# Kernel optimization log

Measured on AMD Instinct MI355X. Metric: run time of the kernel, lower is better.

## Reference

```python
import jax, jax.numpy as jnp
import numpy as np

B, L, C = 2048, 2048, 16
F = L // 2                 # num_freqs = 1024
H = 4 * F                  # multi_factor * num_freqs = 4096
P = int(len(np.unique(L // np.arange(1, F + 1))))  # n patch sizes = 88
SCALE = 0.02
NOISE_EPS = 0.01


def setup_inputs() -> dict:
    key = jax.random.key(0)
    ks = jax.random.split(key, 10)
    return {
        "x": jax.random.normal(ks[0], (B, L, C), jnp.float32),
        "w_start": SCALE * jax.random.normal(ks[1], (C, 1), jnp.float32),
        "b_start": SCALE * jax.random.normal(ks[2], (1,), jnp.float32),
        "w1": SCALE * jax.random.normal(ks[3], (2, F, H), jnp.float32),
        "b1": SCALE * jax.random.normal(ks[4], (2, H), jnp.float32),
        "w2": SCALE * jax.random.normal(ks[5], (2, H, F), jnp.float32),
        "b2": SCALE * jax.random.normal(ks[6], (2, F), jnp.float32),
        "w_gate": SCALE * jax.random.normal(ks[7], (F, P), jnp.float32),
        "w_noise": SCALE * jax.random.normal(ks[8], (F, P), jnp.float32),
        "noise_z": jax.random.normal(ks[9], (B, P), jnp.float32),
        "top_k": 3,
    }


def reference(x, w_start, b_start, w1, b1, w2, b2, w_gate, w_noise, noise_z, top_k):
    # start_fc: [B, L, C] -> [B, L, 1] -> [B, 1, L]
    v = (jnp.einsum("blc,co->blo", x, w_start) + b_start).transpose(0, 2, 1)
    # rfft (ortho), drop DC bin -> [B, 1, F] complex
    xf = jnp.fft.rfft(v, axis=-1, norm="ortho")[:, :, 1:]
    xr, xi = jnp.real(xf), jnp.imag(xf)
    # complex 2-layer MLP in frequency domain
    o1r = jax.nn.relu(jnp.einsum("bdi,io->bdo", xr, w1[0]) - jnp.einsum("bdi,io->bdo", xi, w1[1]) + b1[0])
    o1i = jax.nn.relu(jnp.einsum("bdi,io->bdo", xi, w1[0]) + jnp.einsum("bdi,io->bdo", xr, w1[1]) + b1[1])
    o2r = jnp.einsum("bdo,of->bdf", o1r, w2[0]) - jnp.einsum("bdo,of->bdf", o1i, w2[1]) + b2[0]
    o2i = jnp.einsum("bdo,of->bdf", o1i, w2[0]) + jnp.einsum("bdo,of->bdf", o1r, w2[1]) + b2[1]
    amp = jnp.sqrt(o2r * o2r + o2i * o2i)[:, 0, :]  # [B, F]
    # router logits with (training) noise injection
    clean_logits = amp @ w_gate                      # [B, P]
    noise_std = jax.nn.softplus(amp @ w_noise) + NOISE_EPS
    logits = clean_logits + noise_z * noise_std
    # top-k -> softmax over top-k -> scatter into sparse gates
    top_w, top_i = jax.lax.top_k(logits, top_k)
    top_w = jax.nn.softmax(top_w, axis=-1)
    rows = jnp.arange(logits.shape[0])[:, None]
    gates = jnp.zeros_like(logits).at[rows, top_i].set(top_w)
    return gates
```

## Files before the change

kernel.cpp:

```cpp
#include <hip/hip_runtime.h>
#include <hip/hip_bf16.h>
#include <math.h>

#define B_DIM 2048
#define L_DIM 2048
#define F_DIM 1024
#define H_DIM 4096
#define P_DIM 88

typedef unsigned short u16;
typedef short bf16x8 __attribute__((ext_vector_type(8)));
typedef float f32x4 __attribute__((ext_vector_type(4)));

__device__ __forceinline__ u16 f2bf(float x) {
    unsigned u = __float_as_uint(x);
    return (u16)((u + 0x7fffu + ((u >> 16) & 1u)) >> 16);
}
__device__ __forceinline__ float bf2f(u16 h) {
    return __uint_as_float(((unsigned)h) << 16);
}

__device__ __forceinline__ void gload_lds16(const void* g, void* l) {
    unsigned loff = (unsigned)(uintptr_t)l;
    __builtin_amdgcn_global_load_lds(
        reinterpret_cast<const __attribute__((address_space(1))) void*>(
            reinterpret_cast<uintptr_t>(g)),
        reinterpret_cast<__attribute__((address_space(3))) void*>(loff),
        16, 0, 0);
}

__global__ __launch_bounds__(256) void fft_kernel(
    const float* __restrict__ x, const float* __restrict__ w_start,
    const float* __restrict__ b_start, u16* __restrict__ A1)
{
    __shared__ float re[2048];
    __shared__ float im[2048];
    __shared__ float twr[1024];
    __shared__ float twi[1024];
    int b = blockIdx.x;
    const size_t row0 = (size_t)(2 * b) * 2048;

    const float4* wp = (const float4*)w_start;
    float4 w0 = wp[0], w1 = wp[1], w2 = wp[2], w3 = wp[3];
    float bs = b_start[0];

    for (int i = threadIdx.x; i < 1024; i += 256) {
        float ang = -6.283185307179586f * ((float)i / 2048.0f);
        sincosf(ang, &twi[i], &twr[i]);
    }

    for (int l = threadIdx.x; l < 2048; l += 256) {
        const float4* xp0 = (const float4*)(x + (row0 + l) * 16);
        const float4* xp1 = (const float4*)(x + (row0 + 2048 + l) * 16);
        float4 a0 = xp0[0], a1 = xp0[1], a2 = xp0[2], a3 = xp0[3];
        float4 c0 = xp1[0], c1 = xp1[1], c2 = xp1[2], c3 = xp1[3];
        float va = bs, vb = bs;
        va += a0.x * w0.x + a0.y * w0.y + a0.z * w0.z + a0.w * w0.w;
        va += a1.x * w1.x + a1.y * w1.y + a1.z * w1.z + a1.w * w1.w;
        va += a2.x * w2.x + a2.y * w2.y + a2.z * w2.z + a2.w * w2.w;
        va += a3.x * w3.x + a3.y * w3.y + a3.z * w3.z + a3.w * w3.w;
        vb += c0.x * w0.x + c0.y * w0.y + c0.z * w0.z + c0.w * w0.w;
        vb += c1.x * w1.x + c1.y * w1.y + c1.z * w1.z + c1.w * w1.w;
        vb += c2.x * w2.x + c2.y * w2.y + c2.z * w2.z + c2.w * w2.w;
        vb += c3.x * w3.x + c3.y * w3.y + c3.z * w3.z + c3.w * w3.w;
        unsigned j = __brev((unsigned)l) >> 21;
        re[j] = va;
        im[j] = vb;
    }
    __syncthreads();

    for (int s = 1; s <= 11; s++) {
        int half = 1 << (s - 1);
        for (int t = threadIdx.x; t < 1024; t += 256) {
            int j = t & (half - 1);
            int base = (t >> (s - 1)) << s;
            int idx = j << (11 - s);
            float wr = twr[idx], wi = twi[idx];
            int i0 = base + j, i1 = i0 + half;
            float br = re[i1], bi = im[i1];
            float tr = br * wr - bi * wi;
            float ti = br * wi + bi * wr;
            float ar = re[i0], ai = im[i0];
            re[i0] = ar + tr; im[i0] = ai + ti;
            re[i1] = ar - tr; im[i1] = ai - ti;
        }
        __syncthreads();
    }

    const float sc = 0.5f * 0.022097086912079612f;
    u16* r0 = A1 + (size_t)(2 * b) * 4096;
    u16* r1 = r0 + 4096;
    for (int t = threadIdx.x; t < 1024; t += 256) {
        int k = t + 1;
        int nk = 2048 - k;
        float Zr = re[k], Zi = im[k], Yr = re[nk], Yi = im[nk];
        float Ar = (Zr + Yr) * sc;
        float Ai = (Zi - Yi) * sc;
        float Br = (Zi + Yi) * sc;
        float Bi = (Yr - Zr) * sc;
        u16 h, lo;
        h = f2bf(Ar); lo = f2bf(Ar - bf2f(h)); r0[t] = h; r0[1024 + t] = lo;
        h = f2bf(Ai); lo = f2bf(Ai - bf2f(h)); r0[2048 + t] = h; r0[3072 + t] = lo;
        h = f2bf(Br); lo = f2bf(Br - bf2f(h)); r1[t] = h; r1[1024 + t] = lo;
        h = f2bf(Bi); lo = f2bf(Bi - bf2f(h)); r1[2048 + t] = h; r1[3072 + t] = lo;
    }
}

__global__ __launch_bounds__(256) void conv_bt_kernel(
    const float* __restrict__ w, u16* __restrict__ BT, int Kc, int Nh)
{
    __shared__ float t0[32][33];
    __shared__ float t1[32][33];
    int k0 = blockIdx.x * 32, n0 = blockIdx.y * 32;
    int tx = threadIdx.x, ty = threadIdx.y;
    const float* w0 = w;
    const float* w1 = w + (size_t)Kc * Nh;

#pragma unroll
    for (int i = 0; i < 4; i++) {
        int k = k0 + ty + 8 * i;
        t0[ty + 8 * i][tx] = w0[(size_t)k * Nh + n0 + tx];
        t1[ty + 8 * i][tx] = w1[(size_t)k * Nh + n0 + tx];
    }
    __syncthreads();

    size_t K4 = 4 * (size_t)Kc;
    int k = k0 + tx;
#pragma unroll
    for (int i = 0; i < 4; i++) {
        int nl = ty + 8 * i;
        int n = n0 + nl;
        float br = t0[tx][nl];
        float bi = t1[tx][nl];
        u16 brh = f2bf(br); u16 brl = f2bf(br - bf2f(brh));
        float nbi = -bi;
        u16 nih = f2bf(nbi); u16 nil = f2bf(nbi - bf2f(nih));
        u16 pih = f2bf(bi);  u16 pil = f2bf(bi - bf2f(pih));
        u16* rowr = BT + (size_t)n * K4;
        rowr[0 * Kc + k] = brh; rowr[1 * Kc + k] = brl;
        rowr[2 * Kc + k] = nih; rowr[3 * Kc + k] = nil;
        u16* rowi = BT + (size_t)(Nh + n) * K4;
        rowi[0 * Kc + k] = pih; rowi[1 * Kc + k] = pil;
        rowi[2 * Kc + k] = brh; rowi[3 * Kc + k] = brl;
    }
}

extern __shared__ char smem8p[];

#define MFMA16(ACC0, ACC1, ACC2, ACC3, A0, A1, A2, A3, B0, B1, B2, B3)           \
    ACC0[0] = __builtin_amdgcn_mfma_f32_16x16x32_bf16(A0, B0, ACC0[0], 0, 0, 0); \
    ACC0[1] = __builtin_amdgcn_mfma_f32_16x16x32_bf16(A0, B1, ACC0[1], 0, 0, 0); \
    ACC0[2] = __builtin_amdgcn_mfma_f32_16x16x32_bf16(A0, B2, ACC0[2], 0, 0, 0); \
    ACC0[3] = __builtin_amdgcn_mfma_f32_16x16x32_bf16(A0, B3, ACC0[3], 0, 0, 0); \
    ACC1[0] = __builtin_amdgcn_mfma_f32_16x16x32_bf16(A1, B0, ACC1[0], 0, 0, 0); \
    ACC1[1] = __builtin_amdgcn_mfma_f32_16x16x32_bf16(A1, B1, ACC1[1], 0, 0, 0); \
    ACC1[2] = __builtin_amdgcn_mfma_f32_16x16x32_bf16(A1, B2, ACC1[2], 0, 0, 0); \
    ACC1[3] = __builtin_amdgcn_mfma_f32_16x16x32_bf16(A1, B3, ACC1[3], 0, 0, 0); \
    ACC2[0] = __builtin_amdgcn_mfma_f32_16x16x32_bf16(A2, B0, ACC2[0], 0, 0, 0); \
    ACC2[1] = __builtin_amdgcn_mfma_f32_16x16x32_bf16(A2, B1, ACC2[1], 0, 0, 0); \
    ACC2[2] = __builtin_amdgcn_mfma_f32_16x16x32_bf16(A2, B2, ACC2[2], 0, 0, 0); \
    ACC2[3] = __builtin_amdgcn_mfma_f32_16x16x32_bf16(A2, B3, ACC2[3], 0, 0, 0); \
    ACC3[0] = __builtin_amdgcn_mfma_f32_16x16x32_bf16(A3, B0, ACC3[0], 0, 0, 0); \
    ACC3[1] = __builtin_amdgcn_mfma_f32_16x16x32_bf16(A3, B1, ACC3[1], 0, 0, 0); \
    ACC3[2] = __builtin_amdgcn_mfma_f32_16x16x32_bf16(A3, B2, ACC3[2], 0, 0, 0); \
    ACC3[3] = __builtin_amdgcn_mfma_f32_16x16x32_bf16(A3, B3, ACC3[3], 0, 0, 0);

template <int EPI, int SWZ>
__global__ __launch_bounds__(512, 2) void gemm8p(
    const u16* __restrict__ A, const u16* __restrict__ B,
    const float* __restrict__ biasL, const float* __restrict__ biasR,
    u16* __restrict__ OutU, float* __restrict__ P01, float* __restrict__ P23,
    int Kc, int KcLog, int NH, int nt)
{
    char* ldsA = smem8p;
    char* ldsB = smem8p + 65536;

    const int tid = threadIdx.x;
    const int w = tid >> 6, lane = tid & 63;
    const int wr = w >> 2, wc = w & 3;
    const int fr = lane & 15, kb = lane >> 4;

    int bx, by, z;
    if (SWZ) {
        int b = blockIdx.x;
        int xcd = b & 7, idx = b >> 3;
        bx = 4 * xcd + (idx & 3);
        by = idx >> 2;
        z = 0;
    } else {
        bx = blockIdx.x; by = blockIdx.y; z = blockIdx.z;
    }
    const int n0 = bx * 256, m0 = by * 256;
    const size_t K4 = 4 * (size_t)Kc;

    const int srow = tid >> 2;
    const int lk8 = (((tid & 3) ^ ((tid >> 3) & 3))) * 8;
    const int wb = (tid >> 6) * 1024;

    const int laneOff = fr * 64 + ((kb ^ ((fr >> 1) & 3)) << 4);

    f32x4 acc[8][4];
#pragma unroll
    for (int i = 0; i < 8; i++)
#pragma unroll
        for (int j = 0; j < 4; j++)
            acc[i][j] = (f32x4){0.f, 0.f, 0.f, 0.f};

    const int t0 = z * nt, te = t0 + nt;

    auto colA = [&](int t) {
        int k0 = t << 5;
        int seg = k0 >> KcLog, kk = k0 & (Kc - 1);
        int r3 = seg >= 3 ? seg - 3 : seg;
        int bs = seg >= 3 ? 2 : 0;
        return (bs + (r3 == 1 ? 1 : 0)) * Kc + kk;
    };
    auto colB = [&](int t) {
        int k0 = t << 5;
        int seg = k0 >> KcLog, kk = k0 & (Kc - 1);
        int r3 = seg >= 3 ? seg - 3 : seg;
        int bs = seg >= 3 ? 2 : 0;
        return (bs + (r3 == 2 ? 1 : 0)) * Kc + kk;
    };
    auto stageA = [&](int t) {
        const u16* src = A + (size_t)(m0 + srow) * K4 + colA(t) + lk8;
        char* dst = ldsA + (t & 3) * 16384 + wb;
        gload_lds16(src, dst);
        gload_lds16(src + (size_t)128 * K4, dst + 8192);
    };
    auto stageB = [&](int t) {
        const u16* src = B + (size_t)(n0 + srow) * K4 + colB(t) + lk8;
        char* dst = ldsB + (t & 3) * 16384 + wb;
        gload_lds16(src, dst);
        gload_lds16(src + (size_t)128 * K4, dst + 8192);
    };
    auto aBase = [&](int t) -> const char* {
        return ldsA + (t & 3) * 16384 + wr * 8192 + laneOff;
    };
    auto bBase = [&](int t) -> const char* {
        return ldsB + (t & 3) * 16384 + wc * 4096 + laneOff;
    };

    stageA(t0); stageB(t0);
    if (t0 + 1 < te) {
        stageA(t0 + 1); stageB(t0 + 1);
        asm volatile("s_waitcnt vmcnt(4)" ::: "memory");
    } else {
        asm volatile("s_waitcnt vmcnt(0)" ::: "memory");
    }
    asm volatile("s_barrier" ::: "memory");

    for (int t = t0; t < te; ++t) {
        const bool s2 = (t + 2 < te);
        const char* aS = aBase(t);
        const char* bS = bBase(t);

        bf16x8 a0 = *(const bf16x8*)(aS + 0 * 1024);
        bf16x8 a1 = *(const bf16x8*)(aS + 1 * 1024);
        bf16x8 a2 = *(const bf16x8*)(aS + 2 * 1024);
        bf16x8 a3 = *(const bf16x8*)(aS + 3 * 1024);
        bf16x8 b0 = *(const bf16x8*)(bS + 0 * 1024);
        bf16x8 b1 = *(const bf16x8*)(bS + 1 * 1024);
        bf16x8 b2 = *(const bf16x8*)(bS + 2 * 1024);
        bf16x8 b3 = *(const bf16x8*)(bS + 3 * 1024);
        if (s2) stageA(t + 2);
        asm volatile("s_barrier" ::: "memory");
        asm volatile("s_waitcnt lgkmcnt(0)" ::: "memory");
        __builtin_amdgcn_sched_barrier(0);
        __builtin_amdgcn_s_setprio(1);
        MFMA16(acc[0], acc[1], acc[2], acc[3], a0, a1, a2, a3, b0, b1, b2, b3)
        __builtin_amdgcn_s_setprio(0);
        asm volatile("s_barrier" ::: "memory");

        bf16x8 c0 = *(const bf16x8*)(aS + 4096 + 0 * 1024);
        bf16x8 c1 = *(const bf16x8*)(aS + 4096 + 1 * 1024);
        bf16x8 c2 = *(const bf16x8*)(aS + 4096 + 2 * 1024);
        bf16x8 c3 = *(const bf16x8*)(aS + 4096 + 3 * 1024);
        if (s2) {
            stageB(t + 2);
            asm volatile("s_waitcnt vmcnt(4)" ::: "memory");
        } else {
            asm volatile("s_waitcnt vmcnt(0)" ::: "memory");
        }
        asm volatile("s_barrier" ::: "memory");
        asm volatile("s_waitcnt lgkmcnt(0)" ::: "memory");
        __builtin_amdgcn_sched_barrier(0);
        __builtin_amdgcn_s_setprio(1);
        MFMA16(acc[4], acc[5], acc[6], acc[7], c0, c1, c2, c3, b0, b1, b2, b3)
        __builtin_amdgcn_s_setprio(0);
        asm volatile("s_barrier" ::: "memory");
    }

    const int fq = kb;
#pragma unroll
    for (int nj = 0; nj < 4; nj++) {
        int n = n0 + wc * 64 + nj * 16 + fr;
        if (EPI == 0) {
            bool left = (n < NH);
            int nn = left ? n : (n - NH);
            float bias = left ? biasL[n] : biasR[nn];
#pragma unroll
            for (int mi = 0; mi < 8; mi++) {
                int mb = m0 + wr * 128 + mi * 16 + fq * 4;
#pragma unroll
                for (int r = 0; r < 4; r++) {
                    float val = fmaxf(acc[mi][nj][r] + bias, 0.f);
                    u16 h = f2bf(val);
                    u16 lo = f2bf(val - bf2f(h));
                    size_t rb = (size_t)(mb + r) * (4 * (size_t)NH);
                    if (left) { OutU[rb + nn] = h; OutU[rb + NH + nn] = lo; }
                    else { OutU[rb + 2 * (size_t)NH + nn] = h; OutU[rb + 3 * (size_t)NH + nn] = lo; }
                }
            }
        } else {
            const size_t PSZ = (size_t)2048 * 2048;
            float* Out = (z < 2) ? (P01 + (size_t)z * PSZ) : (P23 + (size_t)(z - 2) * PSZ);
#pragma unroll
            for (int mi = 0; mi < 8; mi++) {
                int mb = m0 + wr * 128 + mi * 16 + fq * 4;
#pragma unroll
                for (int r = 0; r < 4; r++)
                    Out[(size_t)(mb + r) * 2048 + n] = acc[mi][nj][r];
            }
        }
    }
}

__global__ __launch_bounds__(256) void router_kernel(
    const float* __restrict__ P01, const float* __restrict__ P23, int ZK,
    const float* __restrict__ b2,
    const float* __restrict__ w_gate, const float* __restrict__ w_noise,
    const float* __restrict__ noise_z, float* __restrict__ gates)
{
    __shared__ float s_amp[8][1024];
    __shared__ float s_dot[8][176];
    __shared__ float s_lg[8][88];
    __shared__ int   s_idx[8][3];
    __shared__ float s_val[8][3];

    const int tid = threadIdx.x;
    const int r0 = blockIdx.x * 8;
    const size_t PSZ = (size_t)2048 * 2048;

    for (int idx = tid; idx < 8 * 1024; idx += 256) {
        int row = idx >> 10, i = idx & 1023;
        size_t roff = (size_t)(r0 + row) * 2048;
        float orr = b2[i];
        float oii = b2[1024 + i];
        for (int zz = 0; zz < ZK; zz++) {
            const float* Pz = ((zz < 2) ? (P01 + (size_t)zz * PSZ)
                                        : (P23 + (size_t)(zz - 2) * PSZ)) + roff;
            orr += Pz[i];
            oii += Pz[1024 + i];
        }
        s_amp[row][i] = sqrtf(orr * orr + oii * oii);
    }
    __syncthreads();

    for (int idx = tid; idx < 8 * 176; idx += 256) {
        int row = idx / 176, c = idx % 176;
        const float* wcol = (c < 88) ? (w_gate + c) : (w_noise + (c - 88));
        float s = 0.f;
        const float4* av = (const float4*)s_amp[row];
        for (int k4 = 0; k4 < 256; k4++) {
            float4 a = av[k4];
            int k = k4 * 4;
            s = fmaf(a.x, wcol[(size_t)(k + 0) * 88], s);
            s = fmaf(a.y, wcol[(size_t)(k + 1) * 88], s);
            s = fmaf(a.z, wcol[(size_t)(k + 2) * 88], s);
            s = fmaf(a.w, wcol[(size_t)(k + 3) * 88], s);
        }
        s_dot[row][c] = s;
    }
    __syncthreads();

    for (int idx = tid; idx < 8 * 88; idx += 256) {
        int row = idx / 88, c = idx % 88;
        float cn = s_dot[row][88 + c];
        float ns = (cn > 20.f) ? cn : log1pf(expf(cn));
        ns += 0.01f;
        s_lg[row][c] = s_dot[row][c] + noise_z[(size_t)(r0 + row) * 88 + c] * ns;
    }
    __syncthreads();

    if (tid < 8) {
        int i0 = -1, i1 = -1, i2 = -1;
        float v0 = -1e30f, v1 = -1e30f, v2 = -1e30f;
        for (int i = 0; i < P_DIM; i++) {
            float t = s_lg[tid][i];
            if (t > v0) { v0 = t; i0 = i; }
        }
        for (int i = 0; i < P_DIM; i++) {
            if (i == i0) continue;
            float t = s_lg[tid][i];
            if (t > v1) { v1 = t; i1 = i; }
        }
        for (int i = 0; i < P_DIM; i++) {
            if (i == i0 || i == i1) continue;
            float t = s_lg[tid][i];
            if (t > v2) { v2 = t; i2 = i; }
        }
        s_idx[tid][0] = i0; s_idx[tid][1] = i1; s_idx[tid][2] = i2;
        s_val[tid][0] = v0; s_val[tid][1] = v1; s_val[tid][2] = v2;
    }
    __syncthreads();

    for (int idx = tid; idx < 8 * 88; idx += 256) {
        int row = idx / 88, c = idx % 88;
        float m = s_val[row][0];
        float e0 = expf(s_val[row][0] - m);
        float e1 = expf(s_val[row][1] - m);
        float e2 = expf(s_val[row][2] - m);
        float inv = 1.f / (e0 + e1 + e2);
        float g = 0.f;
        if (c == s_idx[row][0]) g = e0 * inv;
        else if (c == s_idx[row][1]) g = e1 * inv;
        else if (c == s_idx[row][2]) g = e2 * inv;
        gates[(size_t)(r0 + row) * 88 + c] = g;
    }
}

extern "C" void kernel_launch(void* const* d_in, const int* in_sizes, int n_in,
                              void* d_out, int out_size, void* d_ws, size_t ws_size,
                              hipStream_t stream)
{
    const float* x       = (const float*)d_in[0];
    const float* w_start = (const float*)d_in[1];
    const float* b_start = (const float*)d_in[2];
    const float* w1      = (const float*)d_in[3];
    const float* b1      = (const float*)d_in[4];
    const float* w2      = (const float*)d_in[5];
    const float* b2      = (const float*)d_in[6];
    const float* w_gate  = (const float*)d_in[7];
    const float* w_noise = (const float*)d_in[8];
    const float* noise_z = (const float*)d_in[9];
    float* gates = (float*)d_out;

    const size_t MB = 1024 * 1024;
    char* base = (char*)d_ws;
    u16*  A1   = (u16*)(base + 16 * MB);
    u16*  BT   = (u16*)(base + 32 * MB);
    u16*  A2   = (u16*)(base + 96 * MB);
    float* P01 = (float*)base;
    float* P23 = (float*)(base + 160 * MB);

    int ZK = (ws_size >= (size_t)192 * MB) ? 4 : 2;

    hipFuncSetAttribute(reinterpret_cast<const void*>(&gemm8p<0, 1>),
                        hipFuncAttributeMaxDynamicSharedMemorySize, 131072);
    hipFuncSetAttribute(reinterpret_cast<const void*>(&gemm8p<1, 0>),
                        hipFuncAttributeMaxDynamicSharedMemorySize, 131072);

    fft_kernel<<<B_DIM / 2, 256, 0, stream>>>(x, w_start, b_start, A1);

    conv_bt_kernel<<<dim3(F_DIM / 32, H_DIM / 32), dim3(32, 8), 0, stream>>>(
        w1, BT, F_DIM, H_DIM);
    gemm8p<0, 1><<<256, 512, 131072, stream>>>(
        A1, BT, b1, b1 + H_DIM, A2, nullptr, nullptr, F_DIM, 10, H_DIM, 192);

    conv_bt_kernel<<<dim3(H_DIM / 32, F_DIM / 32), dim3(32, 8), 0, stream>>>(
        w2, BT, H_DIM, F_DIM);
    gemm8p<1, 0><<<dim3(8, 8, ZK), 512, 131072, stream>>>(
        A2, BT, nullptr, nullptr, nullptr, P01, P23, H_DIM, 12, F_DIM, 768 / ZK);

    router_kernel<<<B_DIM / 8, 256, 0, stream>>>(
        P01, P23, ZK, b2, w_gate, w_noise, noise_z, gates);
}
```

Measured before the change: 634.9 us.

## Switch GEMM to 32x32x16 MFMA with register double-buffered LDS reads

Replaces the 16x16x32 bf16 MFMA tiling (8x4 accumulators per wave) with 32x32x16 MFMA (4x2 f32x16 accumulators). It also restructures the main loop into a software pipeline. The next tile's first-half operands are prefetched into registers while the current second-half MFMAs run, and both A and B stage loads are issued together, leaving one barrier per iteration instead of four. The aim is fewer LDS reads per FLOP and less synchronisation stall. The risks are higher register pressure from the prefetched operands and new LDS read patterns that may cause bank conflicts.

Measured after the change: 618.0 us. -2.7%, faster.

```diff
diff --git a/kernel.cpp b/kernel.cpp
--- a/kernel.cpp
+++ b/kernel.cpp
@@ -11,6 +11,7 @@
 typedef unsigned short u16;
 typedef short bf16x8 __attribute__((ext_vector_type(8)));
 typedef float f32x4 __attribute__((ext_vector_type(4)));
+typedef float f32x16 __attribute__((ext_vector_type(16)));
 
 __device__ __forceinline__ u16 f2bf(float x) {
     unsigned u = __float_as_uint(x);
@@ -147,23 +148,8 @@
 
 extern __shared__ char smem8p[];
 
-#define MFMA16(ACC0, ACC1, ACC2, ACC3, A0, A1, A2, A3, B0, B1, B2, B3)           \
-    ACC0[0] = __builtin_amdgcn_mfma_f32_16x16x32_bf16(A0, B0, ACC0[0], 0, 0, 0); \
-    ACC0[1] = __builtin_amdgcn_mfma_f32_16x16x32_bf16(A0, B1, ACC0[1], 0, 0, 0); \
-    ACC0[2] = __builtin_amdgcn_mfma_f32_16x16x32_bf16(A0, B2, ACC0[2], 0, 0, 0); \
-    ACC0[3] = __builtin_amdgcn_mfma_f32_16x16x32_bf16(A0, B3, ACC0[3], 0, 0, 0); \
-    ACC1[0] = __builtin_amdgcn_mfma_f32_16x16x32_bf16(A1, B0, ACC1[0], 0, 0, 0); \
-    ACC1[1] = __builtin_amdgcn_mfma_f32_16x16x32_bf16(A1, B1, ACC1[1], 0, 0, 0); \
-    ACC1[2] = __builtin_amdgcn_mfma_f32_16x16x32_bf16(A1, B2, ACC1[2], 0, 0, 0); \
-    ACC1[3] = __builtin_amdgcn_mfma_f32_16x16x32_bf16(A1, B3, ACC1[3], 0, 0, 0); \
-    ACC2[0] = __builtin_amdgcn_mfma_f32_16x16x32_bf16(A2, B0, ACC2[0], 0, 0, 0); \
-    ACC2[1] = __builtin_amdgcn_mfma_f32_16x16x32_bf16(A2, B1, ACC2[1], 0, 0, 0); \
-    ACC2[2] = __builtin_amdgcn_mfma_f32_16x16x32_bf16(A2, B2, ACC2[2], 0, 0, 0); \
-    ACC2[3] = __builtin_amdgcn_mfma_f32_16x16x32_bf16(A2, B3, ACC2[3], 0, 0, 0); \
-    ACC3[0] = __builtin_amdgcn_mfma_f32_16x16x32_bf16(A3, B0, ACC3[0], 0, 0, 0); \
-    ACC3[1] = __builtin_amdgcn_mfma_f32_16x16x32_bf16(A3, B1, ACC3[1], 0, 0, 0); \
-    ACC3[2] = __builtin_amdgcn_mfma_f32_16x16x32_bf16(A3, B2, ACC3[2], 0, 0, 0); \
-    ACC3[3] = __builtin_amdgcn_mfma_f32_16x16x32_bf16(A3, B3, ACC3[3], 0, 0, 0);
+#define MFMA32(D, A_, B_) \
+    D = __builtin_amdgcn_mfma_f32_32x32x16_bf16(A_, B_, D, 0, 0, 0)
 
 template <int EPI, int SWZ>
 __global__ __launch_bounds__(512, 2) void gemm8p(
@@ -178,7 +164,7 @@
     const int tid = threadIdx.x;
     const int w = tid >> 6, lane = tid & 63;
     const int wr = w >> 2, wc = w & 3;
-    const int fr = lane & 15, kb = lane >> 4;
+    const int l31 = lane & 31, hi = lane >> 5;
 
     int bx, by, z;
     if (SWZ) {
@@ -197,14 +183,15 @@
     const int lk8 = (((tid & 3) ^ ((tid >> 3) & 3))) * 8;
     const int wb = (tid >> 6) * 1024;
 
-    const int laneOff = fr * 64 + ((kb ^ ((fr >> 1) & 3)) << 4);
-
-    f32x4 acc[8][4];
-#pragma unroll
-    for (int i = 0; i < 8; i++)
-#pragma unroll
-        for (int j = 0; j < 4; j++)
-            acc[i][j] = (f32x4){0.f, 0.f, 0.f, 0.f};
+    const int xsw = (l31 >> 1) & 3;
+    const int laneOff = l31 * 64 + ((hi ^ xsw) << 4);
+
+    f32x16 acc[4][2];
+#pragma unroll
+    for (int i = 0; i < 4; i++)
+#pragma unroll
+        for (int j = 0; j < 2; j++)
+            acc[i][j] = (f32x16)(0.f);
 
     const int t0 = z * nt, te = t0 + nt;
 
@@ -234,11 +221,13 @@
         gload_lds16(src, dst);
         gload_lds16(src + (size_t)128 * K4, dst + 8192);
     };
-    auto aBase = [&](int t) -> const char* {
-        return ldsA + (t & 3) * 16384 + wr * 8192 + laneOff;
-    };
-    auto bBase = [&](int t) -> const char* {
-        return ldsB + (t & 3) * 16384 + wc * 4096 + laneOff;
+    auto aRd = [&](int t, int mt, int s) -> bf16x8 {
+        return *(const bf16x8*)(ldsA + (t & 3) * 16384 + wr * 8192 +
+                                mt * 2048 + (laneOff ^ (s << 5)));
+    };
+    auto bRd = [&](int t, int ntt, int s) -> bf16x8 {
+        return *(const bf16x8*)(ldsB + (t & 3) * 16384 + wc * 4096 +
+                                ntt * 2048 + (laneOff ^ (s << 5)));
     };
 
     stageA(t0); stageB(t0);
@@ -250,64 +239,61 @@
     }
     asm volatile("s_barrier" ::: "memory");
 
+    bf16x8 a0 = aRd(t0, 0, 0), a1 = aRd(t0, 1, 0);
+    bf16x8 a2 = aRd(t0, 2, 0), a3 = aRd(t0, 3, 0);
+    bf16x8 b0 = bRd(t0, 0, 0), b1 = bRd(t0, 1, 0);
+
     for (int t = t0; t < te; ++t) {
-        const bool s2 = (t + 2 < te);
-        const char* aS = aBase(t);
-        const char* bS = bBase(t);
-
-        bf16x8 a0 = *(const bf16x8*)(aS + 0 * 1024);
-        bf16x8 a1 = *(const bf16x8*)(aS + 1 * 1024);
-        bf16x8 a2 = *(const bf16x8*)(aS + 2 * 1024);
-        bf16x8 a3 = *(const bf16x8*)(aS + 3 * 1024);
-        bf16x8 b0 = *(const bf16x8*)(bS + 0 * 1024);
-        bf16x8 b1 = *(const bf16x8*)(bS + 1 * 1024);
-        bf16x8 b2 = *(const bf16x8*)(bS + 2 * 1024);
-        bf16x8 b3 = *(const bf16x8*)(bS + 3 * 1024);
-        if (s2) stageA(t + 2);
+        const bool haveStage = (t + 2 < te);
+        const bool haveNext  = (t + 1 < te);
+
+        if (haveStage) { stageA(t + 2); stageB(t + 2); }
+
+        bf16x8 c0 = aRd(t, 0, 1), c1 = aRd(t, 1, 1);
+        bf16x8 c2 = aRd(t, 2, 1), c3 = aRd(t, 3, 1);
+        bf16x8 d0 = bRd(t, 0, 1), d1 = bRd(t, 1, 1);
+
+        __builtin_amdgcn_s_setprio(1);
+        MFMA32(acc[0][0], a0, b0); MFMA32(acc[0][1], a0, b1);
+        MFMA32(acc[1][0], a1, b0); MFMA32(acc[1][1], a1, b1);
+        MFMA32(acc[2][0], a2, b0); MFMA32(acc[2][1], a2, b1);
+        MFMA32(acc[3][0], a3, b0); MFMA32(acc[3][1], a3, b1);
+        __builtin_amdgcn_s_setprio(0);
+
+        if (haveStage) asm volatile("s_waitcnt vmcnt(4)" ::: "memory");
+        else           asm volatile("s_waitcnt vmcnt(0)" ::: "memory");
         asm volatile("s_barrier" ::: "memory");
-        asm volatile("s_waitcnt lgkmcnt(0)" ::: "memory");
-        __builtin_amdgcn_sched_barrier(0);
+
+        if (haveNext) {
+            a0 = aRd(t + 1, 0, 0); a1 = aRd(t + 1, 1, 0);
+            a2 = aRd(t + 1, 2, 0); a3 = aRd(t + 1, 3, 0);
+            b0 = bRd(t + 1, 0, 0); b1 = bRd(t + 1, 1, 0);
+        }
+
         __builtin_amdgcn_s_setprio(1);
-        MFMA16(acc[0], acc[1], acc[2], acc[3], a0, a1, a2, a3, b0, b1, b2, b3)
+        MFMA32(acc[0][0], c0, d0); MFMA32(acc[0][1], c0, d1);
+        MFMA32(acc[1][0], c1, d0); MFMA32(acc[1][1], c1, d1);
+        MFMA32(acc[2][0], c2, d0); MFMA32(acc[2][1], c2, d1);
+        MFMA32(acc[3][0], c3, d0); MFMA32(acc[3][1], c3, d1);
         __builtin_amdgcn_s_setprio(0);
-        asm volatile("s_barrier" ::: "memory");
-
-        bf16x8 c0 = *(const bf16x8*)(aS + 4096 + 0 * 1024);
-        bf16x8 c1 = *(const bf16x8*)(aS + 4096 + 1 * 1024);
-        bf16x8 c2 = *(const bf16x8*)(aS + 4096 + 2 * 1024);
-        bf16x8 c3 = *(const bf16x8*)(aS + 4096 + 3 * 1024);
-        if (s2) {
-            stageB(t + 2);
-            asm volatile("s_waitcnt vmcnt(4)" ::: "memory");
-        } else {
-            asm volatile("s_waitcnt vmcnt(0)" ::: "memory");
-        }
-        asm volatile("s_barrier" ::: "memory");
-        asm volatile("s_waitcnt lgkmcnt(0)" ::: "memory");
-        __builtin_amdgcn_sched_barrier(0);
-        __builtin_amdgcn_s_setprio(1);
-        MFMA16(acc[4], acc[5], acc[6], acc[7], c0, c1, c2, c3, b0, b1, b2, b3)
-        __builtin_amdgcn_s_setprio(0);
-        asm volatile("s_barrier" ::: "memory");
-    }
-
-    const int fq = kb;
-#pragma unroll
-    for (int nj = 0; nj < 4; nj++) {
-        int n = n0 + wc * 64 + nj * 16 + fr;
+    }
+
+#pragma unroll
+    for (int ntt = 0; ntt < 2; ntt++) {
+        int n = n0 + wc * 64 + ntt * 32 + l31;
         if (EPI == 0) {
             bool left = (n < NH);
             int nn = left ? n : (n - NH);
             float bias = left ? biasL[n] : biasR[nn];
 #pragma unroll
-            for (int mi = 0; mi < 8; mi++) {
-                int mb = m0 + wr * 128 + mi * 16 + fq * 4;
-#pragma unroll
-                for (int r = 0; r < 4; r++) {
-                    float val = fmaxf(acc[mi][nj][r] + bias, 0.f);
+            for (int mt = 0; mt < 4; mt++) {
+#pragma unroll
+                for (int q = 0; q < 16; q++) {
+                    int m = m0 + wr * 128 + mt * 32 + (q & 3) + 8 * (q >> 2) + 4 * hi;
+                    float val = fmaxf(acc[mt][ntt][q] + bias, 0.f);
                     u16 h = f2bf(val);
                     u16 lo = f2bf(val - bf2f(h));
-                    size_t rb = (size_t)(mb + r) * (4 * (size_t)NH);
+                    size_t rb = (size_t)m * (4 * (size_t)NH);
                     if (left) { OutU[rb + nn] = h; OutU[rb + NH + nn] = lo; }
                     else { OutU[rb + 2 * (size_t)NH + nn] = h; OutU[rb + 3 * (size_t)NH + nn] = lo; }
                 }
@@ -316,11 +302,12 @@
             const size_t PSZ = (size_t)2048 * 2048;
             float* Out = (z < 2) ? (P01 + (size_t)z * PSZ) : (P23 + (size_t)(z - 2) * PSZ);
 #pragma unroll
-            for (int mi = 0; mi < 8; mi++) {
-                int mb = m0 + wr * 128 + mi * 16 + fq * 4;
-#pragma unroll
-                for (int r = 0; r < 4; r++)
-                    Out[(size_t)(mb + r) * 2048 + n] = acc[mi][nj][r];
+            for (int mt = 0; mt < 4; mt++) {
+#pragma unroll
+                for (int q = 0; q < 16; q++) {
+                    int m = m0 + wr * 128 + mt * 32 + (q & 3) + 8 * (q >> 2) + 4 * hi;
+                    Out[(size_t)m * 2048 + n] = acc[mt][ntt][q];
+                }
             }
         }
     }
```

## Software-pipeline LDS fragment reads and cut barriers in bf16 MFMA GEMM loop

Applied to the files above, without the earlier changes.

The main K loop of the MFMA GEMM is restructured. A and B fragments for the next tile are read from LDS while the current tile's MFMAs run, global-to-LDS staging for both operands is issued together at the top of each iteration, and the four barriers per iteration drop to one. This relies on the 4-deep LDS ring buffer to avoid overwrite hazards. The second GEMM also moves to a 1D grid with a remapped block order (m-block fastest, then n, then split-K) to change which tiles run together and how caches are reused. The risks are higher register pressure from the held fragments and ordering hazards on shared LDS buffers.

Measured after the change: 600.5 us. -5.4%, faster.

```diff
diff --git a/kernel.cpp b/kernel.cpp
--- a/kernel.cpp
+++ b/kernel.cpp
@@ -181,12 +181,18 @@
     const int fr = lane & 15, kb = lane >> 4;
 
     int bx, by, z;
-    if (SWZ) {
+    if (SWZ == 1) {
         int b = blockIdx.x;
         int xcd = b & 7, idx = b >> 3;
         bx = 4 * xcd + (idx & 3);
         by = idx >> 2;
         z = 0;
+    } else if (SWZ == 2) {
+        int b = blockIdx.x;
+        by = b & 7;
+        int s = b >> 3;
+        bx = s & 7;
+        z = s >> 3;
     } else {
         bx = blockIdx.x; by = blockIdx.y; z = blockIdx.z;
     }
@@ -242,53 +248,64 @@
     };
 
     stageA(t0); stageB(t0);
-    if (t0 + 1 < te) {
-        stageA(t0 + 1); stageB(t0 + 1);
-        asm volatile("s_waitcnt vmcnt(4)" ::: "memory");
-    } else {
-        asm volatile("s_waitcnt vmcnt(0)" ::: "memory");
-    }
+    if (t0 + 1 < te) { stageA(t0 + 1); stageB(t0 + 1); }
+    if (t0 + 1 < te) asm volatile("s_waitcnt vmcnt(4)" ::: "memory");
+    else             asm volatile("s_waitcnt vmcnt(0)" ::: "memory");
     asm volatile("s_barrier" ::: "memory");
 
+    bf16x8 b0, b1, b2, b3, a0, a1, a2, a3;
+    {
+        const char* aS = aBase(t0);
+        const char* bS = bBase(t0);
+        b0 = *(const bf16x8*)(bS + 0 * 1024);
+        b1 = *(const bf16x8*)(bS + 1 * 1024);
+        b2 = *(const bf16x8*)(bS + 2 * 1024);
+        b3 = *(const bf16x8*)(bS + 3 * 1024);
+        a0 = *(const bf16x8*)(aS + 0 * 1024);
+        a1 = *(const bf16x8*)(aS + 1 * 1024);
+        a2 = *(const bf16x8*)(aS + 2 * 1024);
+        a3 = *(const bf16x8*)(aS + 3 * 1024);
+    }
+
     for (int t = t0; t < te; ++t) {
-        const bool s2 = (t + 2 < te);
+        const bool haveStage = (t + 2 < te);
+        const bool haveNext  = (t + 1 < te);
+
+        if (haveStage) { stageA(t + 2); stageB(t + 2); }
+
         const char* aS = aBase(t);
-        const char* bS = bBase(t);
-
-        bf16x8 a0 = *(const bf16x8*)(aS + 0 * 1024);
-        bf16x8 a1 = *(const bf16x8*)(aS + 1 * 1024);
-        bf16x8 a2 = *(const bf16x8*)(aS + 2 * 1024);
-        bf16x8 a3 = *(const bf16x8*)(aS + 3 * 1024);
-        bf16x8 b0 = *(const bf16x8*)(bS + 0 * 1024);
-        bf16x8 b1 = *(const bf16x8*)(bS + 1 * 1024);
-        bf16x8 b2 = *(const bf16x8*)(bS + 2 * 1024);
-        bf16x8 b3 = *(const bf16x8*)(bS + 3 * 1024);
-        if (s2) stageA(t + 2);
-        asm volatile("s_barrier" ::: "memory");
-        asm volatile("s_waitcnt lgkmcnt(0)" ::: "memory");
-        __builtin_amdgcn_sched_barrier(0);
-        __builtin_amdgcn_s_setprio(1);
-        MFMA16(acc[0], acc[1], acc[2], acc[3], a0, a1, a2, a3, b0, b1, b2, b3)
-        __builtin_amdgcn_s_setprio(0);
-        asm volatile("s_barrier" ::: "memory");
-
         bf16x8 c0 = *(const bf16x8*)(aS + 4096 + 0 * 1024);
         bf16x8 c1 = *(const bf16x8*)(aS + 4096 + 1 * 1024);
         bf16x8 c2 = *(const bf16x8*)(aS + 4096 + 2 * 1024);
         bf16x8 c3 = *(const bf16x8*)(aS + 4096 + 3 * 1024);
-        if (s2) {
-            stageB(t + 2);
-            asm volatile("s_waitcnt vmcnt(4)" ::: "memory");
-        } else {
-            asm volatile("s_waitcnt vmcnt(0)" ::: "memory");
-        }
+
+        __builtin_amdgcn_s_setprio(1);
+        MFMA16(acc[0], acc[1], acc[2], acc[3], a0, a1, a2, a3, b0, b1, b2, b3)
+        __builtin_amdgcn_s_setprio(0);
+
+        if (haveStage) asm volatile("s_waitcnt vmcnt(4)" ::: "memory");
+        else           asm volatile("s_waitcnt vmcnt(0)" ::: "memory");
         asm volatile("s_barrier" ::: "memory");
-        asm volatile("s_waitcnt lgkmcnt(0)" ::: "memory");
-        __builtin_amdgcn_sched_barrier(0);
+
+        if (haveNext) {
+            const char* aN = aBase(t + 1);
+            a0 = *(const bf16x8*)(aN + 0 * 1024);
+            a1 = *(const bf16x8*)(aN + 1 * 1024);
+            a2 = *(const bf16x8*)(aN + 2 * 1024);
+            a3 = *(const bf16x8*)(aN + 3 * 1024);
+        }
+
         __builtin_amdgcn_s_setprio(1);
         MFMA16(acc[4], acc[5], acc[6], acc[7], c0, c1, c2, c3, b0, b1, b2, b3)
         __builtin_amdgcn_s_setprio(0);
-        asm volatile("s_barrier" ::: "memory");
+
+        if (haveNext) {
+            const char* bN = bBase(t + 1);
+            b0 = *(const bf16x8*)(bN + 0 * 1024);
+            b1 = *(const bf16x8*)(bN + 1 * 1024);
+            b2 = *(const bf16x8*)(bN + 2 * 1024);
+            b3 = *(const bf16x8*)(bN + 3 * 1024);
+        }
     }
 
     const int fq = kb;
@@ -448,7 +465,7 @@
 
     hipFuncSetAttribute(reinterpret_cast<const void*>(&gemm8p<0, 1>),
                         hipFuncAttributeMaxDynamicSharedMemorySize, 131072);
-    hipFuncSetAttribute(reinterpret_cast<const void*>(&gemm8p<1, 0>),
+    hipFuncSetAttribute(reinterpret_cast<const void*>(&gemm8p<1, 2>),
                         hipFuncAttributeMaxDynamicSharedMemorySize, 131072);
 
     fft_kernel<<<B_DIM / 2, 256, 0, stream>>>(x, w_start, b_start, A1);
@@ -460,7 +477,7 @@
 
     conv_bt_kernel<<<dim3(H_DIM / 32, F_DIM / 32), dim3(32, 8), 0, stream>>>(
         w2, BT, H_DIM, F_DIM);
-    gemm8p<1, 0><<<dim3(8, 8, ZK), 512, 131072, stream>>>(
+    gemm8p<1, 2><<<64 * ZK, 512, 131072, stream>>>(
         A2, BT, nullptr, nullptr, nullptr, P01, P23, H_DIM, 12, F_DIM, 768 / ZK);
 
     router_kernel<<<B_DIM / 8, 256, 0, stream>>>(
```
